# Kernel tuning notes

Hardware: AMD Instinct MI355X
Metric: run time of the kernel (lower is better)

The kernel has to match this reference:

```python
import jax, jax.numpy as jnp
import numpy as np

N = 1024      # num nodes
E = 16384     # num edges
P = 8192      # num query pairs
HD1 = 64      # hidden_dim_1
HD2 = 64      # hidden_dim_2
VOCAB = 1000  # max_x + 1
EPS = 1e-5


def gcn_conv(x, W, b, src, dst, n):
    # PyG GCNConv: h = D^{-1/2} (A + I) D^{-1/2} (x @ W) + b
    h = x @ W
    loop = jnp.arange(n)
    s = jnp.concatenate([src, loop])
    d = jnp.concatenate([dst, loop])
    deg = jnp.zeros((n,), h.dtype).at[d].add(1.0)
    dis = jax.lax.rsqrt(deg)  # deg >= 1 due to self-loops
    norm = dis[s] * dis[d]
    out = jnp.zeros_like(h).at[d].add(norm[:, None] * h[s])
    return out + b


def graph_norm(x, w, b, alpha):
    # PyG GraphNorm with a single graph: stats over node dim (axis 0)
    mean = jnp.mean(x, axis=0, keepdims=True)
    sh = x - alpha * mean
    var = jnp.mean(sh * sh, axis=0, keepdims=True)
    return w * sh / jnp.sqrt(var + EPS) + b


def _forward(x_ids, ei, pos, emb, gW0, gb0, gnw0, gnb0, gna0, gW1, gb1,
             gnw1, gnb1, gna1, m1W, m1b, m2W, m2b, m3W, m3b,
             gn3w, gn3b, gn3a, ldW, ldb):
    n = x_ids.shape[0]
    src, dst = ei[0], ei[1]
    x = emb[x_ids]                                            # [n, HD1]
    # 1-WL: two GCNConv -> GraphNorm -> ReLU blocks
    x = jax.nn.relu(graph_norm(gcn_conv(x, gW0, gb0, src, dst, n), gnw0, gnb0, gna0))
    x = jax.nn.relu(graph_norm(gcn_conv(x, gW1, gb1, src, dst, n), gnw1, gnb1, gna1))
    # O(n^2) outer product: X[i,j] = x[i] * x[j]
    X = x[:, None, :] * x[None, :, :]                         # [n, n, HD1]
    eim = jnp.zeros((n, n), x.dtype).at[src, dst].set(1.0)    # adjacency indicator
    # add_chan = eye(n) @ eim = eim
    X = jnp.concatenate([X, eim[:, :, None]], axis=-1)        # [n, n, HD1+1]
    # 2-FWL refinement (layer2 = 1)
    x1 = jax.nn.relu(X @ m1W + m1b)                           # [n, n, HD2]
    x2 = jax.nn.relu(X @ m2W + m2b)                           # [n, n, HD2]
    prod = jnp.einsum('ikc,kjc->ijc', x1, x2)                 # per-channel bmm
    X = jnp.concatenate([X, prod], axis=-1)                   # [n, n, HD1+1+HD2]
    X = jax.nn.relu(graph_norm(X @ m3W + m3b, gn3w, gn3b, gn3a))
    # symmetric mul-pool then gather query pairs
    X = X * jnp.transpose(X, (1, 0, 2))                       # [n, n, HD2]
    feat = X[pos[:, 0], pos[:, 1]]                            # [P, HD2]
    return feat @ ldW + ldb                                   # [P, 1]


def setup_inputs() -> dict:
    key = jax.random.key(0)
    ks = jax.random.split(key, 12)
    sc = lambda k, s: jax.random.normal(k, s, jnp.float32) * 0.05
    d = {}
    d['x_ids'] = jax.random.randint(ks[0], (N,), 0, VOCAB)
    d['ei'] = jax.random.randint(ks[1], (2, E), 0, N)
    d['pos'] = jax.random.randint(ks[2], (P, 2), 0, N)
    d['emb'] = sc(ks[3], (VOCAB, HD1))
    d['gW0'] = sc(ks[4], (HD1, HD1)); d['gb0'] = jnp.zeros((HD1,), jnp.float32)
    d['gnw0'] = jnp.ones((HD1,), jnp.float32); d['gnb0'] = jnp.zeros((HD1,), jnp.float32); d['gna0'] = jnp.ones((HD1,), jnp.float32)
    d['gW1'] = sc(ks[5], (HD1, HD1)); d['gb1'] = jnp.zeros((HD1,), jnp.float32)
    d['gnw1'] = jnp.ones((HD1,), jnp.float32); d['gnb1'] = jnp.zeros((HD1,), jnp.float32); d['gna1'] = jnp.ones((HD1,), jnp.float32)
    d['m1W'] = sc(ks[6], (HD1 + 1, HD2)); d['m1b'] = jnp.zeros((HD2,), jnp.float32)
    d['m2W'] = sc(ks[7], (HD1 + 1, HD2)); d['m2b'] = jnp.zeros((HD2,), jnp.float32)
    d['m3W'] = sc(ks[8], (HD2 + HD1 + 1, HD2)); d['m3b'] = jnp.zeros((HD2,), jnp.float32)
    d['gn3w'] = jnp.ones((HD2,), jnp.float32); d['gn3b'] = jnp.zeros((HD2,), jnp.float32); d['gn3a'] = jnp.ones((HD2,), jnp.float32)
    d['ldW'] = sc(ks[9], (HD2, 1)); d['ldb'] = jnp.zeros((1,), jnp.float32)
    return d


def reference(x_ids, ei, pos, emb, gW0, gb0, gnw0, gnb0, gna0, gW1, gb1,
              gnw1, gnb1, gna1, m1W, m1b, m2W, m2b, m3W, m3b,
              gn3w, gn3b, gn3a, ldW, ldb):
    return _forward(x_ids, ei, pos, emb, gW0, gb0, gnw0, gnb0, gna0, gW1, gb1,
                    gnw1, gnb1, gna1, m1W, m1b, m2W, m2b, m3W, m3b,
                    gn3w, gn3b, gn3a, ldW, ldb)
```

## Files before the change

kernel.cpp:

```cpp
#include <hip/hip_runtime.h>


typedef unsigned short u16;
typedef unsigned int u32;

#define DI static __device__ __forceinline__

DI float bf2f(u16 u) { union { u32 i; float f; } v; v.i = ((u32)u) << 16; return v.f; }
DI u16 f2bf(float f) {
  union { float f; u32 i; } v; v.f = f;
  u32 u = v.i;
  return (u16)((u + 0x7fffu + ((u >> 16) & 1u)) >> 16);
}

typedef __bf16 bf16x8 __attribute__((ext_vector_type(8)));
typedef float f32x4 __attribute__((ext_vector_type(4)));

#define MFMA16(a, b, c) __builtin_amdgcn_mfma_f32_16x16x32_bf16((a), (b), (c), 0, 0, 0)

typedef const __attribute__((address_space(1))) u32* gas1;
typedef __attribute__((address_space(3))) u32* las3;


__global__ void k_setup(const int* __restrict__ xids, const float* __restrict__ emb,
                        float* __restrict__ xf, float* __restrict__ deg,
                        u32* __restrict__ eimu) {
  int g = blockIdx.x * 256 + threadIdx.x;
  if (g < 262144) eimu[g] = 0u;
  if (g < 1024) deg[g] = 1.0f;
  if (g < 65536) {
    int i = g >> 6, d = g & 63;
    xf[g] = emb[xids[i] * 64 + d];
  }
}

__global__ void k_edges(const int* __restrict__ ei, float* __restrict__ deg,
                        unsigned char* __restrict__ eim) {
  int e = blockIdx.x * 256 + threadIdx.x;
  if (e < 16384) {
    int s = ei[e], d = ei[16384 + e];
    atomicAdd(&deg[d], 1.0f);
    eim[s * 1024 + d] = 1;
  }
}

__global__ void k_gemm_node(const float* __restrict__ xf, const float* __restrict__ W,
                            const float* __restrict__ gb, const float* __restrict__ deg,
                            float* __restrict__ h, float* __restrict__ agg) {
  __shared__ float xrow[64];
  int i = blockIdx.x, c = threadIdx.x;
  xrow[c] = xf[i * 64 + c];
  __syncthreads();
  float s = 0.f;
#pragma unroll
  for (int d = 0; d < 64; ++d) s += xrow[d] * W[d * 64 + c];
  h[i * 64 + c] = s;
  agg[i * 64 + c] = s / deg[i] + gb[c];
}

__global__ void k_agg(const int* __restrict__ ei, const float* __restrict__ deg,
                      const float* __restrict__ h, float* __restrict__ agg) {
  int g = blockIdx.x * 256 + threadIdx.x;
  int e = g >> 6, c = g & 63;
  int s = ei[e], d = ei[16384 + e];
  float nrm = rsqrtf(deg[s]) * rsqrtf(deg[d]);
  atomicAdd(&agg[d * 64 + c], nrm * h[s * 64 + c]);
}

__global__ void k_gnorm(const float* __restrict__ agg, const float* __restrict__ gw,
                        const float* __restrict__ gbb, const float* __restrict__ ga,
                        float* __restrict__ xf, u16* __restrict__ xb, int last) {
  int c = blockIdx.x, t = threadIdx.x;
  float s = 0.f, ss = 0.f;
  for (int i = t; i < 1024; i += 256) {
    float v = agg[i * 64 + c];
    s += v; ss += v * v;
  }
  __shared__ float Ls[256], Lss[256];
  Ls[t] = s; Lss[t] = ss;
  __syncthreads();
  for (int off = 128; off > 0; off >>= 1) {
    if (t < off) { Ls[t] += Ls[t + off]; Lss[t] += Lss[t + off]; }
    __syncthreads();
  }
  float m = Ls[0] * (1.f / 1024.f);
  float a = ga[c];
  float var = Lss[0] * (1.f / 1024.f) - (2.f * a - a * a) * m * m;
  float sc = gw[c] * rsqrtf(fmaxf(var, 0.f) + 1e-5f);
  float bb = gbb[c];
  for (int i = t; i < 1024; i += 256) {
    float v = agg[i * 64 + c];
    float y = fmaxf(sc * (v - a * m) + bb, 0.f);
    xf[i * 64 + c] = y;
    if (last) xb[i * 64 + c] = f2bf(y);
  }
}

__global__ __launch_bounds__(256, 2) void k_build12(
    const u16* __restrict__ xbg, const unsigned char* __restrict__ eim,
    const float* __restrict__ m1W, const float* __restrict__ m1b,
    const float* __restrict__ m2W, const float* __restrict__ m2b,
    u16* __restrict__ x1tg, u16* __restrict__ x2tg, int cbase) {
  __shared__ u16 As[128 * 80];
  __shared__ u16 Bs[128 * 80];
  __shared__ u16 Cs[64 * 140];
  __shared__ unsigned char El[128 * 132];
  __shared__ float wsc[64];
  int b = blockIdx.x;
  int cg = b & 3;
  int rest = b >> 2;
  int which = rest >> 6;
  int t6 = rest & 63;
  int rbase = (t6 >> 3) * 128, sbase = (t6 & 7) * 128;
  const float* W = which ? m2W : m1W;
  const float* bias = which ? m2b : m1b;
  u16* outg = which ? x2tg : x1tg;
  int t = threadIdx.x;
  {
    int row = t >> 1, half = t & 1;
    const u32* gB = (const u32*)(xbg + (sbase + row) * 64 + half * 32);
    u32* dstB = (u32*)&Bs[row * 80 + half * 32];
#pragma unroll
    for (int k = 0; k < 16; ++k) dstB[k] = gB[k];
    int ab = which ? sbase : rbase;
    int bb = which ? rbase : sbase;
    const u32* gE = (const u32*)(eim + (size_t)(ab + row) * 1024 + bb + half * 64);
    u32* dstE = (u32*)&El[row * 132 + half * 64];
#pragma unroll
    for (int k = 0; k < 16; ++k) dstE[k] = gE[k];
  }
  int lane = t & 63, w = t >> 6;
  int q = lane >> 4, r = lane & 15;
  int wr = w >> 1, wc = w & 1;
  for (int ci = 0; ci < 4; ++ci) {
    int cl = cg * 4 + ci;
    int c = cbase + cl;
    if (t < 64) wsc[t] = W[t * 64 + c];
    __syncthreads();
    {
      int row = t >> 1, half = t & 1;
      const u32* ga = (const u32*)(xbg + (rbase + row) * 64 + half * 32);
      u32* dstA = (u32*)&As[row * 80 + half * 32];
#pragma unroll
      for (int k = 0; k < 16; ++k) {
        u32 u = ga[k];
        float f0 = bf2f((u16)(u & 0xffffu)) * wsc[half * 32 + 2 * k];
        float f1 = bf2f((u16)(u >> 16)) * wsc[half * 32 + 2 * k + 1];
        dstA[k] = (u32)f2bf(f0) | ((u32)f2bf(f1) << 16);
      }
    }
    __syncthreads();
    f32x4 z4 = {0.f, 0.f, 0.f, 0.f};
    f32x4 acc[4][4];
#pragma unroll
    for (int mi = 0; mi < 4; ++mi)
#pragma unroll
      for (int ni = 0; ni < 4; ++ni) acc[mi][ni] = z4;
#pragma unroll
    for (int ks = 0; ks < 2; ++ks) {
      bf16x8 af[4], bfr[4];
#pragma unroll
      for (int mi = 0; mi < 4; ++mi)
        af[mi] = *(const bf16x8*)&As[(wr * 64 + mi * 16 + r) * 80 + ks * 32 + q * 8];
#pragma unroll
      for (int ni = 0; ni < 4; ++ni)
        bfr[ni] = *(const bf16x8*)&Bs[(wc * 64 + ni * 16 + r) * 80 + ks * 32 + q * 8];
#pragma unroll
      for (int mi = 0; mi < 4; ++mi)
#pragma unroll
        for (int ni = 0; ni < 4; ++ni) acc[mi][ni] = MFMA16(af[mi], bfr[ni], acc[mi][ni]);
    }
    float w64 = W[64 * 64 + c];
    float bsv = bias[c];
#pragma unroll
    for (int mi = 0; mi < 4; ++mi) {
#pragma unroll
      for (int ni = 0; ni < 4; ++ni) {
        int col = wc * 64 + ni * 16 + r;
#pragma unroll
        for (int tt = 0; tt < 4; ++tt) {
          int row2 = wr * 64 + mi * 16 + q * 4 + tt;
          float e = (float)(which ? El[col * 132 + row2] : El[row2 * 132 + col]);
          acc[mi][ni][tt] = fmaxf(acc[mi][ni][tt] + e * w64 + bsv, 0.f);
        }
      }
    }
    u16* outp = outg + (size_t)cl * 1048576;
#pragma unroll
    for (int p = 0; p < 2; ++p) {
      __syncthreads();
      if (wr == p) {
#pragma unroll
        for (int mi = 0; mi < 4; ++mi)
#pragma unroll
          for (int ni = 0; ni < 4; ++ni) {
            int col = wc * 64 + ni * 16 + r;
#pragma unroll
            for (int tt = 0; tt < 4; ++tt) {
              int lrow = mi * 16 + q * 4 + tt;
              Cs[lrow * 140 + col] = f2bf(acc[mi][ni][tt]);
            }
          }
      }
      __syncthreads();
      {
        int rl = t >> 4, ch = t & 15;
#pragma unroll
        for (int it = 0; it < 4; ++it) {
          int row = it * 16 + rl;
          uint4 v = *(const uint4*)&Cs[row * 140 + ch * 8];
          *(uint4*)(outp + (size_t)(rbase + p * 64 + row) * 1024 + sbase + ch * 8) = v;
        }
      }
    }
  }
}

__global__ __launch_bounds__(256, 4) void k_prodgemm(
    const u16* __restrict__ x1tg, const u16* __restrict__ x2tg,
    u16* __restrict__ prod, int cbase) {
  __shared__ u16 pool[17408];
  int b = blockIdx.x;
  int cl = (b & 7) + ((b >> 9) << 3);
  int tile = (b >> 3) & 63;
  int i0 = (tile >> 3) * 128, j0 = (tile & 7) * 128;
  const u16* Ap = x1tg + (size_t)cl * 1048576;
  const u16* Bp = x2tg + (size_t)cl * 1048576;
  u16* Pp = prod + (size_t)(cbase + cl) * 1048576;
  int t = threadIdx.x, lane = t & 63, w = t >> 6;
  int q = lane >> 4, r = lane & 15;
  int wr = w >> 1, wc = w & 1;
  int lrow = lane >> 3, lcol = (lane & 7) * 8;
  f32x4 z4 = {0.f, 0.f, 0.f, 0.f};
  f32x4 acc[4][4];
#pragma unroll
  for (int mi = 0; mi < 4; ++mi)
#pragma unroll
    for (int ni = 0; ni < 4; ++ni) acc[mi][ni] = z4;
  for (int kk = 0; kk < 1024; kk += 64) {
    __syncthreads();
#pragma unroll
    for (int s8 = 0; s8 < 4; ++s8) {
      int rowbase = w * 32 + s8 * 8;
      int grow = rowbase + lrow;
      __builtin_amdgcn_global_load_lds(
          (gas1)(Ap + (size_t)(i0 + grow) * 1024 + kk + lcol),
          (las3)&pool[rowbase * 64], 16, 0, 0);
      __builtin_amdgcn_global_load_lds(
          (gas1)(Bp + (size_t)(j0 + grow) * 1024 + kk + lcol),
          (las3)&pool[8192 + rowbase * 64], 16, 0, 0);
    }
    __syncthreads();
#pragma unroll
    for (int ks = 0; ks < 2; ++ks) {
      bf16x8 af[4], bfr[4];
#pragma unroll
      for (int mi = 0; mi < 4; ++mi)
        af[mi] = *(const bf16x8*)&pool[(wr * 64 + mi * 16 + r) * 64 + ks * 32 + q * 8];
#pragma unroll
      for (int ni = 0; ni < 4; ++ni)
        bfr[ni] = *(const bf16x8*)&pool[8192 + (wc * 64 + ni * 16 + r) * 64 + ks * 32 + q * 8];
#pragma unroll
      for (int mi = 0; mi < 4; ++mi)
#pragma unroll
        for (int ni = 0; ni < 4; ++ni) acc[mi][ni] = MFMA16(af[mi], bfr[ni], acc[mi][ni]);
    }
  }
  __syncthreads();
#pragma unroll
  for (int mi = 0; mi < 4; ++mi)
#pragma unroll
    for (int ni = 0; ni < 4; ++ni) {
      int col = wc * 64 + ni * 16 + r;
#pragma unroll
      for (int tt = 0; tt < 4; ++tt) {
        int row2 = wr * 64 + mi * 16 + q * 4 + tt;
        pool[row2 * 136 + col] = f2bf(acc[mi][ni][tt]);
      }
    }
  __syncthreads();
  {
    int rseg = t >> 4, cseg = t & 15;
#pragma unroll
    for (int it = 0; it < 8; ++it) {
      int row = it * 16 + rseg;
      uint4 v = *(const uint4*)&pool[row * 136 + cseg * 8];
      *(uint4*)(Pp + (size_t)(i0 + row) * 1024 + j0 + cseg * 8) = v;
    }
  }
}

__global__ __launch_bounds__(256, 3) void k_buildT(
    const u16* __restrict__ xbg, const unsigned char* __restrict__ eim,
    u16* PT, const float* __restrict__ m3W, const float* __restrict__ m3b,
    float* __restrict__ S, float* __restrict__ SS) {
  __shared__ u16 A[64 * 136];
  __shared__ u16 Wt[64 * 136];
  __shared__ u16 scratch[64 * 66];
  __shared__ u16 stg[64 * 72];
  __shared__ unsigned char eimrow[1024];
  __shared__ float xi[64];
  int i = blockIdx.x;
  int t = threadIdx.x, lane = t & 63, w = t >> 6;
  int q = lane >> 4, r = lane & 15;
  {
    int zidx = i * 256 + t;
    if (zidx < 65536) { S[zidx] = 0.f; SS[zidx] = 0.f; }
  }
  if (t < 64) xi[t] = bf2f(xbg[i * 64 + t]);
  ((u32*)eimrow)[t] = ((const u32*)(eim + (size_t)i * 1024))[t];
  {
    int row = t >> 1, half = t & 1;
    int rsrc = row < 64 ? row : row + 1;
    const float4* gw = (const float4*)(m3W + rsrc * 64 + half * 32);
#pragma unroll
    for (int k = 0; k < 8; ++k) {
      float4 f = gw[k];
      Wt[(half * 32 + 4 * k + 0) * 136 + row] = f2bf(f.x);
      Wt[(half * 32 + 4 * k + 1) * 136 + row] = f2bf(f.y);
      Wt[(half * 32 + 4 * k + 2) * 136 + row] = f2bf(f.z);
      Wt[(half * 32 + 4 * k + 3) * 136 + row] = f2bf(f.w);
    }
  }
  float w64c[4], b3c[4];
#pragma unroll
  for (int ni = 0; ni < 4; ++ni) {
    int cc = ni * 16 + r;
    w64c[ni] = m3W[64 * 64 + cc];
    b3c[ni] = m3b[cc];
  }
  int p4 = t >> 2, q4 = t & 3;
  uint4 pva, pvb, xva, xvb;
  {
    const uint4* gp = (const uint4*)(PT + (size_t)p4 * 1048576 + (size_t)i * 1024 + q4 * 16);
    pva = gp[0]; pvb = gp[1];
    const uint4* gx = (const uint4*)(xbg + p4 * 64 + q4 * 16);
    xva = gx[0]; xvb = gx[1];
  }
  for (int jc = 0; jc < 16; ++jc) {
    int j0 = jc * 64;
    asm volatile("s_waitcnt lgkmcnt(0)" ::: "memory");
    __builtin_amdgcn_s_barrier();
    asm volatile("" ::: "memory");
    {
      u32* sw = (u32*)&scratch[p4 * 66 + q4 * 16];
      sw[0] = pva.x; sw[1] = pva.y; sw[2] = pva.z; sw[3] = pva.w;
      sw[4] = pvb.x; sw[5] = pvb.y; sw[6] = pvb.z; sw[7] = pvb.w;
      u32 xv[8] = {xva.x, xva.y, xva.z, xva.w, xvb.x, xvb.y, xvb.z, xvb.w};
      u32* dst = (u32*)&A[p4 * 136 + q4 * 16];
#pragma unroll
      for (int k = 0; k < 8; ++k) {
        u32 u = xv[k];
        float f0 = bf2f((u16)(u & 0xffffu)) * xi[q4 * 16 + 2 * k];
        float f1 = bf2f((u16)(u >> 16)) * xi[q4 * 16 + 2 * k + 1];
        dst[k] = (u32)f2bf(f0) | ((u32)f2bf(f1) << 16);
      }
    }
    if (jc < 15) {
      const uint4* gp = (const uint4*)(PT + (size_t)p4 * 1048576 + (size_t)i * 1024 + (j0 + 64) + q4 * 16);
      pva = gp[0]; pvb = gp[1];
      const uint4* gx = (const uint4*)(xbg + (j0 + 64 + p4) * 64 + q4 * 16);
      xva = gx[0]; xvb = gx[1];
    }
    if (jc > 0) {
      int pl = t >> 3, off = (t & 7) * 8;
#pragma unroll
      for (int k = 0; k < 2; ++k) {
        int plane = k * 32 + pl;
        uint4 v = *(const uint4*)&stg[plane * 72 + off];
        *(uint4*)(PT + (size_t)plane * 1048576 + (size_t)i * 1024 + (j0 - 64) + off) = v;
      }
    }
    asm volatile("s_waitcnt lgkmcnt(0)" ::: "memory");
    __builtin_amdgcn_s_barrier();
    asm volatile("" ::: "memory");
#pragma unroll
    for (int jj2 = 0; jj2 < 8; ++jj2) {
      int jr = w * 16 + jj2 * 2;
      u32 two = *(const u32*)&scratch[lane * 66 + jr];
      A[jr * 136 + 64 + lane] = (u16)(two & 0xffffu);
      A[(jr + 1) * 136 + 64 + lane] = (u16)(two >> 16);
    }
    asm volatile("s_waitcnt lgkmcnt(0)" ::: "memory");
    __builtin_amdgcn_s_barrier();
    asm volatile("" ::: "memory");
    f32x4 z4 = {0.f, 0.f, 0.f, 0.f};
    f32x4 acc[4];
#pragma unroll
    for (int ni = 0; ni < 4; ++ni) acc[ni] = z4;
#pragma unroll
    for (int ks = 0; ks < 4; ++ks) {
      bf16x8 af, bfr[4];
      af = *(const bf16x8*)&A[(w * 16 + r) * 136 + ks * 32 + q * 8];
#pragma unroll
      for (int ni = 0; ni < 4; ++ni)
        bfr[ni] = *(const bf16x8*)&Wt[(ni * 16 + r) * 136 + ks * 32 + q * 8];
#pragma unroll
      for (int ni = 0; ni < 4; ++ni) acc[ni] = MFMA16(af, bfr[ni], acc[ni]);
    }
#pragma unroll
    for (int tt = 0; tt < 4; ++tt) {
      int jj = w * 16 + q * 4 + tt;
      float ev = (float)eimrow[j0 + jj];
#pragma unroll
      for (int ni = 0; ni < 4; ++ni)
        acc[ni][tt] = acc[ni][tt] + ev * w64c[ni] + b3c[ni];
    }
#pragma unroll
    for (int ni = 0; ni < 4; ++ni) {
      int cc = ni * 16 + r;
#pragma unroll
      for (int tt = 0; tt < 4; ++tt) {
        int jj = w * 16 + q * 4 + tt;
        stg[cc * 72 + jj] = f2bf(acc[ni][tt]);
      }
    }
  }
  asm volatile("s_waitcnt lgkmcnt(0)" ::: "memory");
  __builtin_amdgcn_s_barrier();
  asm volatile("" ::: "memory");
  {
    int pl = t >> 3, off = (t & 7) * 8;
#pragma unroll
    for (int k = 0; k < 2; ++k) {
      int plane = k * 32 + pl;
      uint4 v = *(const uint4*)&stg[plane * 72 + off];
      *(uint4*)(PT + (size_t)plane * 1048576 + (size_t)i * 1024 + 960 + off) = v;
    }
  }
}

__global__ void k_stats(const u16* __restrict__ Tg, float* __restrict__ S,
                        float* __restrict__ SS) {
  int b = blockIdx.x;
  int c = b >> 3, ic = b & 7;
  int t = threadIdx.x;
  const u16* base = Tg + (size_t)c * 1048576 + (size_t)ic * 131072 + t * 4;
  float s0 = 0.f, s1 = 0.f, s2 = 0.f, s3 = 0.f;
  float q0 = 0.f, q1 = 0.f, q2 = 0.f, q3 = 0.f;
  for (int ii = 0; ii < 128; ++ii) {
    uint2 u = *(const uint2*)(base + (size_t)ii * 1024);
    float v0 = bf2f((u16)(u.x & 0xffffu)), v1 = bf2f((u16)(u.x >> 16));
    float v2 = bf2f((u16)(u.y & 0xffffu)), v3 = bf2f((u16)(u.y >> 16));
    s0 += v0; q0 += v0 * v0;
    s1 += v1; q1 += v1 * v1;
    s2 += v2; q2 += v2 * v2;
    s3 += v3; q3 += v3 * v3;
  }
  int base2 = c * 1024 + t * 4;
  atomicAdd(&S[base2 + 0], s0);
  atomicAdd(&S[base2 + 1], s1);
  atomicAdd(&S[base2 + 2], s2);
  atomicAdd(&S[base2 + 3], s3);
  atomicAdd(&SS[base2 + 0], q0);
  atomicAdd(&SS[base2 + 1], q1);
  atomicAdd(&SS[base2 + 2], q2);
  atomicAdd(&SS[base2 + 3], q3);
}

__global__ void k_statsfin(const float* __restrict__ S, const float* __restrict__ SS,
                           const float* __restrict__ gn3w, const float* __restrict__ gn3b,
                           const float* __restrict__ gn3a,
                           float* __restrict__ normA, float* __restrict__ normB) {
  int idx = blockIdx.x * 256 + threadIdx.x;
  int c = idx & 63, j = idx >> 6;
  float sum = S[c * 1024 + j];
  float ssum = SS[c * 1024 + j];
  float m = sum * (1.f / 1024.f);
  float a = gn3a[c];
  float var = ssum * (1.f / 1024.f) - (2.f * a - a * a) * m * m;
  float sc = gn3w[c] * rsqrtf(fmaxf(var, 0.f) + 1e-5f);
  normA[idx] = sc;
  normB[idx] = gn3b[c] - sc * a * m;
}

__global__ void k_final(const u16* __restrict__ Tg, const float* __restrict__ normA,
                        const float* __restrict__ normB, const int* __restrict__ pos,
                        const float* __restrict__ ldW, const float* __restrict__ ldb,
                        float* __restrict__ out) {
  int t = threadIdx.x, w = t >> 6, lane = t & 63;
  int p = blockIdx.x * 4 + w;
  int i = pos[2 * p], j = pos[2 * p + 1];
  float t1 = bf2f(Tg[(size_t)lane * 1048576 + (size_t)i * 1024 + j]);
  float y1 = fmaxf(normA[j * 64 + lane] * t1 + normB[j * 64 + lane], 0.f);
  float t2 = bf2f(Tg[(size_t)lane * 1048576 + (size_t)j * 1024 + i]);
  float y2 = fmaxf(normA[i * 64 + lane] * t2 + normB[i * 64 + lane], 0.f);
  float z = y1 * y2 * ldW[lane];
#pragma unroll
  for (int off = 32; off > 0; off >>= 1) z += __shfl_down(z, off, 64);
  if (lane == 0) out[p] = z + ldb[0];
}

extern "C" void kernel_launch(void* const* d_in, const int* in_sizes, int n_in,
                              void* d_out, int out_size, void* d_ws, size_t ws_size,
                              hipStream_t stream) {
  const int* xids   = (const int*)d_in[0];
  const int* ei     = (const int*)d_in[1];
  const int* pos    = (const int*)d_in[2];
  const float* emb  = (const float*)d_in[3];
  const float* gW0  = (const float*)d_in[4];
  const float* gb0  = (const float*)d_in[5];
  const float* gnw0 = (const float*)d_in[6];
  const float* gnb0 = (const float*)d_in[7];
  const float* gna0 = (const float*)d_in[8];
  const float* gW1  = (const float*)d_in[9];
  const float* gb1  = (const float*)d_in[10];
  const float* gnw1 = (const float*)d_in[11];
  const float* gnb1 = (const float*)d_in[12];
  const float* gna1 = (const float*)d_in[13];
  const float* m1W  = (const float*)d_in[14];
  const float* m1b  = (const float*)d_in[15];
  const float* m2W  = (const float*)d_in[16];
  const float* m2b  = (const float*)d_in[17];
  const float* m3W  = (const float*)d_in[18];
  const float* m3b  = (const float*)d_in[19];
  const float* gn3w = (const float*)d_in[20];
  const float* gn3b = (const float*)d_in[21];
  const float* gn3a = (const float*)d_in[22];
  const float* ldW  = (const float*)d_in[23];
  const float* ldb  = (const float*)d_in[24];

  char* ws = (char*)d_ws;
  float* xf   = (float*)(ws + 0);
  float* h    = (float*)(ws + 262144);
  float* agg  = (float*)(ws + 524288);
  float* deg  = (float*)(ws + 786432);
  u16*   xb   = (u16*)(ws + 790528);
  unsigned char* eim = (unsigned char*)(ws + 921600);
  float* normA = (float*)(ws + 1970176);
  float* normB = (float*)(ws + 2232320);
  u16* x1tg = (u16*)(ws + 2494464);
  u16* x2tg = (u16*)(ws + 36048896);
  u16* prod = (u16*)(ws + 69603328);
  float* Sp  = (float*)x1tg;
  float* SSp = Sp + 65536;
  float* out = (float*)d_out;

  k_setup<<<1024, 256, 0, stream>>>(xids, emb, xf, deg, (u32*)eim);
  k_edges<<<64, 256, 0, stream>>>(ei, deg, eim);
  k_gemm_node<<<1024, 64, 0, stream>>>(xf, gW0, gb0, deg, h, agg);
  k_agg<<<4096, 256, 0, stream>>>(ei, deg, h, agg);
  k_gnorm<<<64, 256, 0, stream>>>(agg, gnw0, gnb0, gna0, xf, xb, 0);
  k_gemm_node<<<1024, 64, 0, stream>>>(xf, gW1, gb1, deg, h, agg);
  k_agg<<<4096, 256, 0, stream>>>(ei, deg, h, agg);
  k_gnorm<<<64, 256, 0, stream>>>(agg, gnw1, gnb1, gna1, xf, xb, 1);
  for (int g = 0; g < 4; ++g) {
    k_build12<<<512, 256, 0, stream>>>(xb, eim, m1W, m1b, m2W, m2b, x1tg, x2tg, g * 16);
    k_prodgemm<<<1024, 256, 0, stream>>>(x1tg, x2tg, prod, g * 16);
  }
  k_buildT<<<1024, 256, 0, stream>>>(xb, eim, prod, m3W, m3b, Sp, SSp);
  k_stats<<<512, 256, 0, stream>>>(prod, Sp, SSp);
  k_statsfin<<<256, 256, 0, stream>>>(Sp, SSp, gn3w, gn3b, gn3a, normA, normB);
  k_final<<<2048, 256, 0, stream>>>(prod, normA, normB, pos, ldW, ldb, out);
}
```

Baseline: 508.0 us.

## Rewrite per-channel product GEMM with 256x256 tiles, double-buffered LDS and swizzle

```diff
diff --git a/kernel.cpp b/kernel.cpp
--- a/kernel.cpp
+++ b/kernel.cpp
@@ -216,77 +216,140 @@
   }
 }
 
-__global__ __launch_bounds__(256, 4) void k_prodgemm(
+__global__ __launch_bounds__(512, 2) void k_prodgemm(
     const u16* __restrict__ x1tg, const u16* __restrict__ x2tg,
     u16* __restrict__ prod, int cbase) {
-  __shared__ u16 pool[17408];
+  __shared__ u16 ldsbuf[65536];
   int b = blockIdx.x;
-  int cl = (b & 7) + ((b >> 9) << 3);
-  int tile = (b >> 3) & 63;
-  int i0 = (tile >> 3) * 128, j0 = (tile & 7) * 128;
+  int bp = (b & 7) * 32 + (b >> 3);
+  int cl = bp >> 4, tile = bp & 15;
+  int i0 = (tile >> 2) * 256, j0 = (tile & 3) * 256;
   const u16* Ap = x1tg + (size_t)cl * 1048576;
   const u16* Bp = x2tg + (size_t)cl * 1048576;
   u16* Pp = prod + (size_t)(cbase + cl) * 1048576;
   int t = threadIdx.x, lane = t & 63, w = t >> 6;
-  int q = lane >> 4, r = lane & 15;
-  int wr = w >> 1, wc = w & 1;
-  int lrow = lane >> 3, lcol = (lane & 7) * 8;
+  int q = lane >> 4, r = lane & 15, rx = r & 7;
+  int wm = w >> 2, wn = w & 3;
+  int subrow = lane >> 3, srcslot = (lane & 7) ^ (lane >> 3);
+
+#define STAGE(KT)                                                           \
+  {                                                                         \
+    int pb_ = (KT) & 1;                                                     \
+    _Pragma("unroll")                                                       \
+    for (int j = 0; j < 8; ++j) {                                           \
+      int rg = w * 8 + j;                                                   \
+      if (w < 4) {                                                          \
+        const u16* src = Ap + (size_t)(i0 + rg * 8 + subrow) * 1024 +       \
+                         (KT) * 64 + srcslot * 8;                           \
+        __builtin_amdgcn_global_load_lds(                                   \
+            (gas1)src, (las3)(ldsbuf + pb_ * 16384 + rg * 512), 16, 0, 0);  \
+      } else {                                                              \
+        const u16* src = Bp + (size_t)(j0 + (rg - 32) * 8 + subrow) * 1024 +\
+                         (KT) * 64 + srcslot * 8;                           \
+        __builtin_amdgcn_global_load_lds(                                   \
+            (gas1)src, (las3)(ldsbuf + 32768 + pb_ * 16384 + (rg - 32) * 512),\
+            16, 0, 0);                                                      \
+      }                                                                     \
+    }                                                                       \
+  }
+
   f32x4 z4 = {0.f, 0.f, 0.f, 0.f};
-  f32x4 acc[4][4];
-#pragma unroll
-  for (int mi = 0; mi < 4; ++mi)
-#pragma unroll
-    for (int ni = 0; ni < 4; ++ni) acc[mi][ni] = z4;
-  for (int kk = 0; kk < 1024; kk += 64) {
-    __syncthreads();
-#pragma unroll
-    for (int s8 = 0; s8 < 4; ++s8) {
-      int rowbase = w * 32 + s8 * 8;
-      int grow = rowbase + lrow;
-      __builtin_amdgcn_global_load_lds(
-          (gas1)(Ap + (size_t)(i0 + grow) * 1024 + kk + lcol),
-          (las3)&pool[rowbase * 64], 16, 0, 0);
-      __builtin_amdgcn_global_load_lds(
-          (gas1)(Bp + (size_t)(j0 + grow) * 1024 + kk + lcol),
-          (las3)&pool[8192 + rowbase * 64], 16, 0, 0);
-    }
-    __syncthreads();
-#pragma unroll
-    for (int ks = 0; ks < 2; ++ks) {
-      bf16x8 af[4], bfr[4];
+  f32x4 acc[8][4];
+#pragma unroll
+  for (int mi = 0; mi < 8; ++mi)
+#pragma unroll
+    for (int n = 0; n < 4; ++n) acc[mi][n] = z4;
+  bf16x8 bfr[4];
+
+#define PHASE(MH, KS, FRESHB, PB)                                           \
+  {                                                                         \
+    bf16x8 afr[4];                                                          \
+    _Pragma("unroll")                                                       \
+    for (int mi = 0; mi < 4; ++mi)                                          \
+      afr[mi] = *(const bf16x8*)&ldsbuf[(PB) * 16384 +                      \
+          (wm * 128 + (MH) * 64 + mi * 16 + r) * 64 +                       \
+          ((((KS) * 4 + q) ^ rx) << 3)];                                    \
+    if (FRESHB) {                                                           \
+      _Pragma("unroll")                                                     \
+      for (int n = 0; n < 4; ++n)                                           \
+        bfr[n] = *(const bf16x8*)&ldsbuf[32768 + (PB) * 16384 +             \
+            (wn * 64 + n * 16 + r) * 64 + ((((KS) * 4 + q) ^ rx) << 3)];    \
+    }                                                                       \
+    asm volatile("s_waitcnt lgkmcnt(0)" ::: "memory");                      \
+    __builtin_amdgcn_sched_barrier(0);                                      \
+    __builtin_amdgcn_s_setprio(1);                                          \
+    _Pragma("unroll")                                                       \
+    for (int mi = 0; mi < 4; ++mi)                                          \
+      _Pragma("unroll")                                                     \
+      for (int n = 0; n < 4; ++n)                                           \
+        acc[(MH) * 4 + mi][n] =                                             \
+            MFMA16(afr[mi], bfr[n], acc[(MH) * 4 + mi][n]);                 \
+    __builtin_amdgcn_s_setprio(0);                                          \
+  }
+
+  STAGE(0);
+#pragma unroll 1
+  for (int kt = 0; kt < 16; ++kt) {
+    int pb = kt & 1;
+    if (kt < 15) {
+      STAGE(kt + 1);
+      asm volatile("s_waitcnt vmcnt(8)" ::: "memory");
+    } else {
+      asm volatile("s_waitcnt vmcnt(0)" ::: "memory");
+    }
+    asm volatile("s_waitcnt lgkmcnt(0)" ::: "memory");
+    __builtin_amdgcn_s_barrier();
+    asm volatile("" ::: "memory");
+    PHASE(0, 0, 1, pb);
+    asm volatile("s_waitcnt lgkmcnt(0)" ::: "memory");
+    __builtin_amdgcn_s_barrier();
+    asm volatile("" ::: "memory");
+    PHASE(1, 0, 0, pb);
+    asm volatile("s_waitcnt lgkmcnt(0)" ::: "memory");
+    __builtin_amdgcn_s_barrier();
+    asm volatile("" ::: "memory");
+    PHASE(0, 1, 1, pb);
+    asm volatile("s_waitcnt lgkmcnt(0)" ::: "memory");
+    __builtin_amdgcn_s_barrier();
+    asm volatile("" ::: "memory");
+    PHASE(1, 1, 0, pb);
+    asm volatile("s_waitcnt lgkmcnt(0)" ::: "memory");
+    __builtin_amdgcn_s_barrier();
+    asm volatile("" ::: "memory");
+  }
+#undef PHASE
+#undef STAGE
+
+#pragma unroll 1
+  for (int p = 0; p < 4; ++p) {
+    if (wm == (p >> 1)) {
+      int mh = p & 1;
 #pragma unroll
       for (int mi = 0; mi < 4; ++mi)
-        af[mi] = *(const bf16x8*)&pool[(wr * 64 + mi * 16 + r) * 64 + ks * 32 + q * 8];
-#pragma unroll
-      for (int ni = 0; ni < 4; ++ni)
-        bfr[ni] = *(const bf16x8*)&pool[8192 + (wc * 64 + ni * 16 + r) * 64 + ks * 32 + q * 8];
-#pragma unroll
-      for (int mi = 0; mi < 4; ++mi)
-#pragma unroll
-        for (int ni = 0; ni < 4; ++ni) acc[mi][ni] = MFMA16(af[mi], bfr[ni], acc[mi][ni]);
-    }
-  }
-  __syncthreads();
-#pragma unroll
-  for (int mi = 0; mi < 4; ++mi)
-#pragma unroll
-    for (int ni = 0; ni < 4; ++ni) {
-      int col = wc * 64 + ni * 16 + r;
-#pragma unroll
-      for (int tt = 0; tt < 4; ++tt) {
-        int row2 = wr * 64 + mi * 16 + q * 4 + tt;
-        pool[row2 * 136 + col] = f2bf(acc[mi][ni][tt]);
-      }
-    }
-  __syncthreads();
-  {
-    int rseg = t >> 4, cseg = t & 15;
-#pragma unroll
-    for (int it = 0; it < 8; ++it) {
-      int row = it * 16 + rseg;
-      uint4 v = *(const uint4*)&pool[row * 136 + cseg * 8];
-      *(uint4*)(Pp + (size_t)(i0 + row) * 1024 + j0 + cseg * 8) = v;
-    }
+#pragma unroll
+        for (int n = 0; n < 4; ++n)
+#pragma unroll
+          for (int tt = 0; tt < 4; ++tt) {
+            int lr = mi * 16 + q * 4 + tt;
+            ldsbuf[lr * 264 + wn * 64 + n * 16 + r] =
+                f2bf(acc[mh * 4 + mi][n][tt]);
+          }
+    }
+    asm volatile("s_waitcnt lgkmcnt(0)" ::: "memory");
+    __builtin_amdgcn_s_barrier();
+    asm volatile("" ::: "memory");
+    {
+      int row = t >> 3, sg = t & 7;
+#pragma unroll
+      for (int it = 0; it < 4; ++it) {
+        int cu = sg * 8 + it * 64;
+        uint4 v = *(const uint4*)&ldsbuf[row * 264 + cu];
+        *(uint4*)(Pp + (size_t)(i0 + p * 64 + row) * 1024 + j0 + cu) = v;
+      }
+    }
+    asm volatile("s_waitcnt lgkmcnt(0)" ::: "memory");
+    __builtin_amdgcn_s_barrier();
+    asm volatile("" ::: "memory");
   }
 }
 
@@ -546,7 +609,7 @@
   k_gnorm<<<64, 256, 0, stream>>>(agg, gnw1, gnb1, gna1, xf, xb, 1);
   for (int g = 0; g < 4; ++g) {
     k_build12<<<512, 256, 0, stream>>>(xb, eim, m1W, m1b, m2W, m2b, x1tg, x2tg, g * 16);
-    k_prodgemm<<<1024, 256, 0, stream>>>(x1tg, x2tg, prod, g * 16);
+    k_prodgemm<<<256, 512, 0, stream>>>(x1tg, x2tg, prod, g * 16);
   }
   k_buildT<<<1024, 256, 0, stream>>>(xb, eim, prod, m3W, m3b, Sp, SSp);
   k_stats<<<512, 256, 0, stream>>>(prod, Sp, SSp);
```

New measurement: 644.7 us. 1.27x slower.
